# Optimization experiments

Hardware: AMD Instinct MI355X
Metric: run time of the kernel (lower is better)

The kernel has to match this reference:

```python
import jax, jax.numpy as jnp
import numpy as np

NTYPE = 3
ALPHA = 0.2
E, N, H, D = 100000, 50000, 4, 128


def setup_inputs() -> dict:
    key = jax.random.key(0)
    k1, k2, k3 = jax.random.split(key, 3)
    batch = jax.random.randint(k1, (E, NTYPE), 0, N)
    # forward's broadcast (batch_features + aggregated) requires every node id
    # to appear at least once (torch.unique(batch) must have N entries)
    batch = batch.at[:N, 0].set(jnp.arange(N))
    batch_features = jax.random.normal(k2, (N, D), dtype=jnp.float32)
    att_weights = jax.random.normal(k3, (NTYPE * E, H, NTYPE - 1), dtype=jnp.float32)
    return {"batch": batch, "batch_features": batch_features, "att_weights": att_weights}


def reference(batch, batch_features, att_weights):
    n_nodes, d = batch_features.shape
    # feat block i: gather embeddings of all type-columns except i -> [NTYPE*E, NTYPE-1, D]
    feat = jnp.concatenate(
        [batch_features[batch[:, [j for j in range(NTYPE) if j != i]]] for i in range(NTYPE)],
        axis=0,
    )
    # batched attention matmul: [NTYPE*E, H, NTYPE-1] x [NTYPE*E, NTYPE-1, D] -> [NTYPE*E, H, D]
    att_feat = jnp.einsum('ehk,ekd->ehd', att_weights, feat)
    # block i of att_feat corresponds to node ids batch[:, i] (matches batch.T.flatten())
    batch_nodes = batch.T.reshape(-1)  # [NTYPE*E]
    # per-node scatter-max aggregation (torch.unique returns sorted ids 0..N-1)
    aggregated = jax.ops.segment_max(att_feat, batch_nodes, num_segments=n_nodes)  # [N, H, D]
    out = batch_features[:, None, :] + aggregated  # broadcast residual -> [N, H, D]
    out = jax.nn.leaky_relu(out, negative_slope=ALPHA)  # concat=True branch
    return out.reshape(n_nodes, -1)  # [N, H*D]
```

## Files before the change

kernel.cpp:

```cpp
#include <hip/hip_runtime.h>

#define NTYPE 3
#define H 4
#define D 128
#define ALPHA 0.2f

__global__ void link_kernel(const int* __restrict__ batch,
                            int* __restrict__ head,
                            int4* __restrict__ recs, int E, int M) {
    int t = blockIdx.x * blockDim.x + threadIdx.x;
    if (t >= M) return;
    int i = t / E;
    int r = t - i * E;
    const int* brow = batch + r * NTYPE;
    const int j0 = (i == 0) ? 1 : 0;
    const int j1 = (i == 2) ? 1 : 2;
    const int dest = brow[i];
    const int next = atomicExch(&head[dest], t);
    recs[t] = make_int4(brow[j0], brow[j1], next, 0);
}

__global__ void aggregate_kernel(const float* __restrict__ bfeat,
                                 const float* __restrict__ attw,
                                 const int4* __restrict__ recs,
                                 const int* __restrict__ head,
                                 float* __restrict__ out) {
    const int n = blockIdx.x;
    const int d = threadIdx.x;

    float acc0 = -__builtin_inff(), acc1 = -__builtin_inff();
    float acc2 = -__builtin_inff(), acc3 = -__builtin_inff();

    int k = head[n];
    while (k != -1) {
        const int4 rec = recs[k];
        const float* wr = attw + (long long)k * (H * (NTYPE - 1));
        const float f0 = bfeat[(long long)rec.x * D + d];
        const float f1 = bfeat[(long long)rec.y * D + d];
        acc0 = fmaxf(acc0, fmaf(wr[0], f0, wr[1] * f1));
        acc1 = fmaxf(acc1, fmaf(wr[2], f0, wr[3] * f1));
        acc2 = fmaxf(acc2, fmaf(wr[4], f0, wr[5] * f1));
        acc3 = fmaxf(acc3, fmaf(wr[6], f0, wr[7] * f1));
        k = rec.z;
    }

    const float bres = bfeat[(long long)n * D + d];
    float* o = out + (long long)n * (H * D) + d;
    float v;
    v = bres + acc0; o[0 * D] = v > 0.f ? v : ALPHA * v;
    v = bres + acc1; o[1 * D] = v > 0.f ? v : ALPHA * v;
    v = bres + acc2; o[2 * D] = v > 0.f ? v : ALPHA * v;
    v = bres + acc3; o[3 * D] = v > 0.f ? v : ALPHA * v;
}

extern "C" void kernel_launch(void* const* d_in, const int* in_sizes, int n_in,
                              void* d_out, int out_size, void* d_ws, size_t ws_size,
                              hipStream_t stream) {
    const int* batch   = (const int*)d_in[0];
    const float* bfeat = (const float*)d_in[1];
    const float* attw  = (const float*)d_in[2];
    const int E = in_sizes[0] / NTYPE;
    const int N = in_sizes[1] / D;
    const int M = NTYPE * E;

    int* head  = (int*)d_ws;
    int4* recs = (int4*)(head + N);

    hipMemsetAsync(head, 0xFF, sizeof(int) * (size_t)N, stream);

    link_kernel<<<(M + 255) / 256, 256, 0, stream>>>(batch, head, recs, E, M);
    aggregate_kernel<<<N, D, 0, stream>>>(bfeat, attw, recs, head, (float*)d_out);
}
```

Baseline: 220.3 us.

## Replace linked-list edge chains with CSR via count/scan/scatter and vectorized aggregation

Swaps the atomic-exchange linked list for a counting-sort CSR layout: a count kernel, a single-block exclusive scan and a scatter kernel build contiguous per-node record ranges. The aggregate kernel then walks those ranges without serial pointer chasing. It uses 64 threads handling two features each, unrolls the edge loop by two, loads weights as float4, and writes the output with nontemporal stores. The cost is two extra launches, including a single-block serial scan over N.

```diff
diff --git a/kernel.cpp b/kernel.cpp
--- a/kernel.cpp
+++ b/kernel.cpp
@@ -5,52 +5,140 @@
 #define D 128
 #define ALPHA 0.2f
 
-__global__ void link_kernel(const int* __restrict__ batch,
-                            int* __restrict__ head,
-                            int4* __restrict__ recs, int E, int M) {
-    int t = blockIdx.x * blockDim.x + threadIdx.x;
-    if (t >= M) return;
-    int i = t / E;
-    int r = t - i * E;
-    const int* brow = batch + r * NTYPE;
-    const int j0 = (i == 0) ? 1 : 0;
-    const int j1 = (i == 2) ? 1 : 2;
-    const int dest = brow[i];
-    const int next = atomicExch(&head[dest], t);
-    recs[t] = make_int4(brow[j0], brow[j1], next, 0);
+typedef float f2 __attribute__((ext_vector_type(2)));
+typedef float f4 __attribute__((ext_vector_type(4)));
+
+__global__ void count_kernel(const int* __restrict__ batch,
+                             int* __restrict__ cnt, int E) {
+    int r = blockIdx.x * blockDim.x + threadIdx.x;
+    if (r >= E) return;
+    const int* row = batch + 3 * r;
+    int b0 = row[0], b1 = row[1], b2 = row[2];
+    atomicAdd(&cnt[b0], 1);
+    atomicAdd(&cnt[b1], 1);
+    atomicAdd(&cnt[b2], 1);
 }
 
-__global__ void aggregate_kernel(const float* __restrict__ bfeat,
-                                 const float* __restrict__ attw,
-                                 const int4* __restrict__ recs,
-                                 const int* __restrict__ head,
-                                 float* __restrict__ out) {
+__global__ void __launch_bounds__(1024) scan_kernel(int* __restrict__ cnt, int N) {
+    __shared__ int lds[1024];
+    const int tid = threadIdx.x;
+    const int chunk = (N + 1023) >> 10;
+    const int lo = tid * chunk;
+    const int hi = min(lo + chunk, N);
+
+    int s = 0;
+    for (int i = lo; i < hi; ++i) s += cnt[i];
+    lds[tid] = s;
+    __syncthreads();
+    for (int off = 1; off < 1024; off <<= 1) {
+        int v = (tid >= off) ? lds[tid - off] : 0;
+        __syncthreads();
+        lds[tid] += v;
+        __syncthreads();
+    }
+    int run = lds[tid] - s;
+    for (int i = lo; i < hi; ++i) {
+        int c = cnt[i];
+        cnt[i] = run;
+        run += c;
+    }
+}
+
+__global__ void scatter_kernel(const int* __restrict__ batch,
+                               int* __restrict__ cursor,
+                               int4* __restrict__ recs, int E) {
+    int r = blockIdx.x * blockDim.x + threadIdx.x;
+    if (r >= E) return;
+    const int* row = batch + 3 * r;
+    int b0 = row[0], b1 = row[1], b2 = row[2];
+    int s0 = atomicAdd(&cursor[b0], 1);
+    recs[s0] = make_int4(b1, b2, r, 0);
+    int s1 = atomicAdd(&cursor[b1], 1);
+    recs[s1] = make_int4(b0, b2, E + r, 0);
+    int s2 = atomicAdd(&cursor[b2], 1);
+    recs[s2] = make_int4(b0, b1, 2 * E + r, 0);
+}
+
+__global__ void __launch_bounds__(64)
+aggregate_kernel(const float* __restrict__ bfeat,
+                 const float* __restrict__ attw,
+                 const int4* __restrict__ recs,
+                 const int* __restrict__ cursor,
+                 float* __restrict__ out) {
     const int n = blockIdx.x;
-    const int d = threadIdx.x;
+    const int t = threadIdx.x;
+    const int e = cursor[n];
+    const int s = (n == 0) ? 0 : cursor[n - 1];
 
-    float acc0 = -__builtin_inff(), acc1 = -__builtin_inff();
-    float acc2 = -__builtin_inff(), acc3 = -__builtin_inff();
+    const float NI = -__builtin_inff();
+    f2 acc0 = {NI, NI}, acc1 = {NI, NI}, acc2 = {NI, NI}, acc3 = {NI, NI};
 
-    int k = head[n];
-    while (k != -1) {
-        const int4 rec = recs[k];
-        const float* wr = attw + (long long)k * (H * (NTYPE - 1));
-        const float f0 = bfeat[(long long)rec.x * D + d];
-        const float f1 = bfeat[(long long)rec.y * D + d];
-        acc0 = fmaxf(acc0, fmaf(wr[0], f0, wr[1] * f1));
-        acc1 = fmaxf(acc1, fmaf(wr[2], f0, wr[3] * f1));
-        acc2 = fmaxf(acc2, fmaf(wr[4], f0, wr[5] * f1));
-        acc3 = fmaxf(acc3, fmaf(wr[6], f0, wr[7] * f1));
-        k = rec.z;
+    int k = s;
+    for (; k + 2 <= e; k += 2) {
+        const int4 ra = recs[k];
+        const int4 rb = recs[k + 1];
+        const f2 fa0 = *(const f2*)(bfeat + (size_t)ra.x * D + 2 * t);
+        const f2 fa1 = *(const f2*)(bfeat + (size_t)ra.y * D + 2 * t);
+        const f2 fb0 = *(const f2*)(bfeat + (size_t)rb.x * D + 2 * t);
+        const f2 fb1 = *(const f2*)(bfeat + (size_t)rb.y * D + 2 * t);
+        const f4 wa0 = *(const f4*)(attw + (size_t)ra.z * 8);
+        const f4 wa1 = *(const f4*)(attw + (size_t)ra.z * 8 + 4);
+        const f4 wb0 = *(const f4*)(attw + (size_t)rb.z * 8);
+        const f4 wb1 = *(const f4*)(attw + (size_t)rb.z * 8 + 4);
+
+        acc0.x = fmaxf(acc0.x, fmaf(wa0.x, fa0.x, wa0.y * fa1.x));
+        acc0.y = fmaxf(acc0.y, fmaf(wa0.x, fa0.y, wa0.y * fa1.y));
+        acc1.x = fmaxf(acc1.x, fmaf(wa0.z, fa0.x, wa0.w * fa1.x));
+        acc1.y = fmaxf(acc1.y, fmaf(wa0.z, fa0.y, wa0.w * fa1.y));
+        acc2.x = fmaxf(acc2.x, fmaf(wa1.x, fa0.x, wa1.y * fa1.x));
+        acc2.y = fmaxf(acc2.y, fmaf(wa1.x, fa0.y, wa1.y * fa1.y));
+        acc3.x = fmaxf(acc3.x, fmaf(wa1.z, fa0.x, wa1.w * fa1.x));
+        acc3.y = fmaxf(acc3.y, fmaf(wa1.z, fa0.y, wa1.w * fa1.y));
+
+        acc0.x = fmaxf(acc0.x, fmaf(wb0.x, fb0.x, wb0.y * fb1.x));
+        acc0.y = fmaxf(acc0.y, fmaf(wb0.x, fb0.y, wb0.y * fb1.y));
+        acc1.x = fmaxf(acc1.x, fmaf(wb0.z, fb0.x, wb0.w * fb1.x));
+        acc1.y = fmaxf(acc1.y, fmaf(wb0.z, fb0.y, wb0.w * fb1.y));
+        acc2.x = fmaxf(acc2.x, fmaf(wb1.x, fb0.x, wb1.y * fb1.x));
+        acc2.y = fmaxf(acc2.y, fmaf(wb1.x, fb0.y, wb1.y * fb1.y));
+        acc3.x = fmaxf(acc3.x, fmaf(wb1.z, fb0.x, wb1.w * fb1.x));
+        acc3.y = fmaxf(acc3.y, fmaf(wb1.z, fb0.y, wb1.w * fb1.y));
+    }
+    if (k < e) {
+        const int4 ra = recs[k];
+        const f2 fa0 = *(const f2*)(bfeat + (size_t)ra.x * D + 2 * t);
+        const f2 fa1 = *(const f2*)(bfeat + (size_t)ra.y * D + 2 * t);
+        const f4 wa0 = *(const f4*)(attw + (size_t)ra.z * 8);
+        const f4 wa1 = *(const f4*)(attw + (size_t)ra.z * 8 + 4);
+        acc0.x = fmaxf(acc0.x, fmaf(wa0.x, fa0.x, wa0.y * fa1.x));
+        acc0.y = fmaxf(acc0.y, fmaf(wa0.x, fa0.y, wa0.y * fa1.y));
+        acc1.x = fmaxf(acc1.x, fmaf(wa0.z, fa0.x, wa0.w * fa1.x));
+        acc1.y = fmaxf(acc1.y, fmaf(wa0.z, fa0.y, wa0.w * fa1.y));
+        acc2.x = fmaxf(acc2.x, fmaf(wa1.x, fa0.x, wa1.y * fa1.x));
+        acc2.y = fmaxf(acc2.y, fmaf(wa1.x, fa0.y, wa1.y * fa1.y));
+        acc3.x = fmaxf(acc3.x, fmaf(wa1.z, fa0.x, wa1.w * fa1.x));
+        acc3.y = fmaxf(acc3.y, fmaf(wa1.z, fa0.y, wa1.w * fa1.y));
     }
 
-    const float bres = bfeat[(long long)n * D + d];
-    float* o = out + (long long)n * (H * D) + d;
-    float v;
-    v = bres + acc0; o[0 * D] = v > 0.f ? v : ALPHA * v;
-    v = bres + acc1; o[1 * D] = v > 0.f ? v : ALPHA * v;
-    v = bres + acc2; o[2 * D] = v > 0.f ? v : ALPHA * v;
-    v = bres + acc3; o[3 * D] = v > 0.f ? v : ALPHA * v;
+    const f2 br = *(const f2*)(bfeat + (size_t)n * D + 2 * t);
+    float* o = out + (size_t)n * (H * D) + 2 * t;
+    f2 v;
+
+    v.x = br.x + acc0.x; v.y = br.y + acc0.y;
+    v.x = v.x > 0.f ? v.x : ALPHA * v.x; v.y = v.y > 0.f ? v.y : ALPHA * v.y;
+    __builtin_nontemporal_store(v, (f2*)(o + 0 * D));
+
+    v.x = br.x + acc1.x; v.y = br.y + acc1.y;
+    v.x = v.x > 0.f ? v.x : ALPHA * v.x; v.y = v.y > 0.f ? v.y : ALPHA * v.y;
+    __builtin_nontemporal_store(v, (f2*)(o + 1 * D));
+
+    v.x = br.x + acc2.x; v.y = br.y + acc2.y;
+    v.x = v.x > 0.f ? v.x : ALPHA * v.x; v.y = v.y > 0.f ? v.y : ALPHA * v.y;
+    __builtin_nontemporal_store(v, (f2*)(o + 2 * D));
+
+    v.x = br.x + acc3.x; v.y = br.y + acc3.y;
+    v.x = v.x > 0.f ? v.x : ALPHA * v.x; v.y = v.y > 0.f ? v.y : ALPHA * v.y;
+    __builtin_nontemporal_store(v, (f2*)(o + 3 * D));
 }
 
 extern "C" void kernel_launch(void* const* d_in, const int* in_sizes, int n_in,
@@ -61,13 +149,14 @@
     const float* attw  = (const float*)d_in[2];
     const int E = in_sizes[0] / NTYPE;
     const int N = in_sizes[1] / D;
-    const int M = NTYPE * E;
 
-    int* head  = (int*)d_ws;
-    int4* recs = (int4*)(head + N);
+    int* cursor = (int*)d_ws;
+    size_t rec_off = (((size_t)N * sizeof(int)) + 15) & ~(size_t)15;
+    int4* recs = (int4*)((char*)d_ws + rec_off);
 
-    hipMemsetAsync(head, 0xFF, sizeof(int) * (size_t)N, stream);
-
-    link_kernel<<<(M + 255) / 256, 256, 0, stream>>>(batch, head, recs, E, M);
-    aggregate_kernel<<<N, D, 0, stream>>>(bfeat, attw, recs, head, (float*)d_out);
+    hipMemsetAsync(cursor, 0, sizeof(int) * (size_t)N, stream);
+    count_kernel<<<(E + 255) / 256, 256, 0, stream>>>(batch, cursor, E);
+    scan_kernel<<<1, 1024, 0, stream>>>(cursor, N);
+    scatter_kernel<<<(E + 255) / 256, 256, 0, stream>>>(batch, cursor, recs, E);
+    aggregate_kernel<<<N, 64, 0, stream>>>(bfeat, attw, recs, cursor, (float*)d_out);
 }
```

Measured after the change: 274.4 us. +24.6%, slower.
